# Kernel tuning notes

Hardware: AMD Instinct MI355X
Metric: run time of the kernel (lower is better)

## Reference

```python
import jax, jax.numpy as jnp
import numpy as np

NUM_HEADS = 16

def setup_inputs() -> dict:
    key = jax.random.key(0)
    ks = jax.random.split(key, 8)
    B, S, X, D = 2, 2048, 1, 1024
    scale = 1.0 / np.sqrt(D)
    return {
        "query": jax.random.normal(ks[0], (B, S, X, D), jnp.float32),
        "key": jax.random.normal(ks[1], (B, S, X, D), jnp.float32),
        "value": jax.random.normal(ks[2], (B, S, X, D), jnp.float32),
        "Wq": jax.random.normal(ks[3], (D, D), jnp.float32) * scale,
        "bq": jnp.zeros((D,), jnp.float32),
        "Wk": jax.random.normal(ks[4], (D, D), jnp.float32) * scale,
        "bk": jnp.zeros((D,), jnp.float32),
        "Wv": jax.random.normal(ks[5], (D, D), jnp.float32) * scale,
        "bv": jnp.zeros((D,), jnp.float32),
        "Wo": jax.random.normal(ks[6], (D, D), jnp.float32) * scale,
        "bo": jnp.zeros((D,), jnp.float32),
    }

def _split_heads(x, B, H):
    # [B, S, X, D] -> [B, H, S*X, depth]
    D = x.shape[-1]
    return x.reshape(B, -1, H, D // H).transpose(0, 2, 1, 3)

def reference(query, key, value, Wq, bq, Wk, bk, Wv, bv, Wo, bo):
    B, S, X, D = query.shape
    H = NUM_HEADS
    q = _split_heads(query @ Wq + bq, B, H)   # [B,H,L,dh], L=S*X
    k = _split_heads(key @ Wk + bk, B, H)
    v = _split_heads(value @ Wv + bv, B, H)
    dh = k.shape[-1]
    logits = jnp.einsum("bhqd,bhkd->bhqk", q, k) / jnp.sqrt(jnp.float32(dh))
    attn = jax.nn.softmax(logits, axis=-1)
    out = jnp.einsum("bhqk,bhkd->bhqd", attn, v)   # [B,H,L,dh]
    out = out.transpose(0, 2, 1, 3).reshape(B, S, -1, D)  # [B,S,X,D]
    return out @ Wo + bo
```

## Files before the change

### kernel.cpp

```cpp
#include <hip/hip_runtime.h>
#include <cstdint>
#include <cstddef>

typedef __bf16 bf16x8 __attribute__((ext_vector_type(8)));
typedef float f32x4 __attribute__((ext_vector_type(4)));
typedef float f32x16 __attribute__((ext_vector_type(16)));
typedef unsigned short u16;
typedef unsigned int u32;

static constexpr int Bn = 2;
static constexpr int L  = 2048;
static constexpr int Dm = 1024;
static constexpr int H  = 16;
static constexpr int DH = 64;
static constexpr int M  = Bn * L;

#define SC 0.18033688f

__device__ __forceinline__ u16 f2bf(float f) {
    union { float f; u32 u; } v; v.f = f;
    u32 u = v.u + 0x7FFFu + ((v.u >> 16) & 1u);
    return (u16)(u >> 16);
}

__device__ __forceinline__ void gl2lds16(const void* g, void* l) {
    __builtin_amdgcn_global_load_lds(
        (const __attribute__((address_space(1))) u32*)(uintptr_t)g,
        (__attribute__((address_space(3))) u32*)(uintptr_t)l, 16, 0, 0);
}

__global__ __launch_bounds__(256) void convert_in(
    const float* __restrict__ q, const float* __restrict__ k, const float* __restrict__ v,
    u16* __restrict__ dst)
{
    const float* src = (blockIdx.y == 0) ? q : (blockIdx.y == 1) ? k : v;
    u16* d = dst + (size_t)blockIdx.y * M * Dm;
    const size_t t = (size_t)blockIdx.x * 256 + threadIdx.x;
    const float4* s4 = reinterpret_cast<const float4*>(src) + t * 2;
    float4 f0 = s4[0], f1 = s4[1];
    u16 o[8] = { f2bf(f0.x), f2bf(f0.y), f2bf(f0.z), f2bf(f0.w),
                 f2bf(f1.x), f2bf(f1.y), f2bf(f1.z), f2bf(f1.w) };
    reinterpret_cast<uint4*>(d)[t] = *reinterpret_cast<uint4*>(o);
}

__global__ __launch_bounds__(256) void convert_wt(
    const float* __restrict__ Wq, const float* __restrict__ Wk,
    const float* __restrict__ Wv, const float* __restrict__ Wo,
    u16* __restrict__ dst)
{
    __shared__ u16 Ts[64][72];
    const int z = blockIdx.z;
    const float* W = (z == 0) ? Wq : (z == 1) ? Wk : (z == 2) ? Wv : Wo;
    u16* o = dst + (size_t)z * Dm * Dm;
    const int n0 = blockIdx.x * 64, k0 = blockIdx.y * 64;
    const int tid = threadIdx.x;

    {
        const int kr = tid >> 2, nc = (tid & 3) * 16;
        const float* s = W + (size_t)(k0 + kr) * Dm + n0 + nc;
        const float4* s4 = reinterpret_cast<const float4*>(s);
        float4 a = s4[0], b = s4[1], c = s4[2], d = s4[3];
        u16 t[16] = { f2bf(a.x), f2bf(a.y), f2bf(a.z), f2bf(a.w),
                      f2bf(b.x), f2bf(b.y), f2bf(b.z), f2bf(b.w),
                      f2bf(c.x), f2bf(c.y), f2bf(c.z), f2bf(c.w),
                      f2bf(d.x), f2bf(d.y), f2bf(d.z), f2bf(d.w) };
        *reinterpret_cast<uint4*>(&Ts[kr][nc])     = reinterpret_cast<uint4*>(t)[0];
        *reinterpret_cast<uint4*>(&Ts[kr][nc + 8]) = reinterpret_cast<uint4*>(t)[1];
    }
    __syncthreads();
    {
        const int nr = tid >> 2, kc = (tid & 3) * 16;
        u16 w[16];
        #pragma unroll
        for (int j = 0; j < 16; ++j) w[j] = Ts[kc + j][nr];
        u16* dptr = o + (size_t)(n0 + nr) * Dm + k0 + kc;
        *reinterpret_cast<uint4*>(dptr)     = reinterpret_cast<uint4*>(w)[0];
        *reinterpret_cast<uint4*>(dptr + 8) = reinterpret_cast<uint4*>(w)[1];
    }
}

__global__ __launch_bounds__(256) void gemm_qkv(
    const u16* __restrict__ Abuf, const u16* __restrict__ Wtb,
    const float* __restrict__ bq, const float* __restrict__ bk, const float* __restrict__ bv,
    u16* __restrict__ Qh, u16* __restrict__ Kh, u16* __restrict__ Vh)
{
    __shared__ u16 As[128 * 32];
    __shared__ u16 Bs[128 * 32];
    const int tid = threadIdx.x;
    const int wave = tid >> 6, lane = tid & 63;
    const int quad = lane >> 4, l16 = lane & 15;
    const int wr = wave >> 1, wc = wave & 1;
    const int z = blockIdx.z;
    const u16* A  = Abuf + (size_t)z * M * Dm;
    const u16* Bt = Wtb  + (size_t)z * Dm * Dm;
    const float* bias = (z == 0) ? bq : (z == 1) ? bk : bv;
    u16* out = (z == 0) ? Qh : (z == 1) ? Kh : Vh;
    const int n0 = blockIdx.x * 128, m0 = blockIdx.y * 128;

    const int srow = lane >> 2;
    const int skc  = (lane & 3) * 8;

    f32x4 acc[4][4] = {};

    for (int k0 = 0; k0 < Dm; k0 += 32) {
        __syncthreads();
        #pragma unroll
        for (int i = 0; i < 2; ++i) {
            const int ra = i * 64 + wave * 16;
            gl2lds16(A  + (size_t)(m0 + ra + srow) * Dm + k0 + skc, &As[ra * 32]);
            gl2lds16(Bt + (size_t)(n0 + ra + srow) * Dm + k0 + skc, &Bs[ra * 32]);
        }
        __syncthreads();
        bf16x8 af[4], bf[4];
        #pragma unroll
        for (int t = 0; t < 4; ++t) {
            af[t] = *reinterpret_cast<const bf16x8*>(&As[(wr * 64 + t * 16 + l16) * 32 + quad * 8]);
            bf[t] = *reinterpret_cast<const bf16x8*>(&Bs[(wc * 64 + t * 16 + l16) * 32 + quad * 8]);
        }
        #pragma unroll
        for (int mt = 0; mt < 4; ++mt)
            #pragma unroll
            for (int nt = 0; nt < 4; ++nt)
                acc[mt][nt] = __builtin_amdgcn_mfma_f32_16x16x32_bf16(af[mt], bf[nt], acc[mt][nt], 0, 0, 0);
    }

    const float qscale = (z == 0) ? SC : 1.0f;
    #pragma unroll
    for (int nt = 0; nt < 4; ++nt) {
        const int n = n0 + wc * 64 + nt * 16 + l16;
        const float badd = bias[n];
        const int h = n >> 6, d = n & 63;
        #pragma unroll
        for (int mt = 0; mt < 4; ++mt) {
            #pragma unroll
            for (int r = 0; r < 4; ++r) {
                const int m = m0 + wr * 64 + mt * 16 + quad * 4 + r;
                const int bb = m >> 11, ll = m & 2047;
                out[(((size_t)(bb * H + h)) * L + ll) * DH + d] = f2bf((acc[mt][nt][r] + badd) * qscale);
            }
        }
    }
}

__global__ __launch_bounds__(256) void transpose_v(
    const u16* __restrict__ Vh, u16* __restrict__ Vth)
{
    __shared__ u16 Ts[64][72];
    const int kt = blockIdx.x, h = blockIdx.y, b = blockIdx.z;
    const int tid = threadIdx.x;
    const size_t hb = ((size_t)(b * H + h)) * L * DH;

    {
        const int kr = tid >> 2, dc = (tid & 3) * 16;
        const u16* s = Vh + hb + (size_t)(kt * 64 + kr) * DH + dc;
        *reinterpret_cast<uint4*>(&Ts[kr][dc])     = *reinterpret_cast<const uint4*>(s);
        *reinterpret_cast<uint4*>(&Ts[kr][dc + 8]) = *reinterpret_cast<const uint4*>(s + 8);
    }
    __syncthreads();
    {
        const int dr = tid >> 2, kc = (tid & 3) * 16;
        u16 w[16];
        #pragma unroll
        for (int j = 0; j < 16; ++j) w[j] = Ts[kc + j][dr];
        u16* dptr = Vth + hb + (size_t)dr * L + kt * 64 + kc;
        *reinterpret_cast<uint4*>(dptr)     = reinterpret_cast<uint4*>(w)[0];
        *reinterpret_cast<uint4*>(dptr + 8) = reinterpret_cast<uint4*>(w)[1];
    }
}

__global__ __launch_bounds__(256) void attn(
    const u16* __restrict__ Qh, const u16* __restrict__ Kh,
    const u16* __restrict__ Vth, u16* __restrict__ ctx)
{
    __shared__ u16 KV[2 * 64 * 64];
    __shared__ u16 Os[64 * 72];

    const int tid  = threadIdx.x;
    const int wave = tid >> 6, lane = tid & 63;
    const int l31  = lane & 31, hh = lane >> 5;
    const int qt = blockIdx.x, h = blockIdx.y, b = blockIdx.z;
    const size_t hb = ((size_t)(b * H + h)) * L * DH;

    const int q0 = qt * 128 + wave * 32;

    bf16x8 qf[4];
    {
        const u16* qp = Qh + hb + (size_t)(q0 + l31) * DH + hh * 8;
        #pragma unroll
        for (int c = 0; c < 4; ++c)
            qf[c] = *reinterpret_cast<const bf16x8*>(qp + c * 16);
    }

    const int r_off = lane >> 3;
    const int s_sl  = lane & 7;

    int vbK[2], vbV[2];
    #pragma unroll
    for (int t = 0; t < 2; ++t) {
        const int rr = t * 32 + l31;
        vbK[t] = rr * 128 + ((rr & 7) << 4);
        vbV[t] = 2 * 64 * 64 + rr * 128 + ((rr & 7) << 4);
    }
    const char* ldsb = (const char*)KV;

    float rsum = 0.f;
    f32x16 oacc[2] = {};

    for (int kt = 0; kt < L / 64; ++kt) {
        __syncthreads();
        #pragma unroll
        for (int i = 0; i < 2; ++i) {
            const int rr = wave * 16 + i * 8 + r_off;
            gl2lds16(Kh  + hb + (size_t)(kt * 64 + rr) * DH + ((s_sl ^ (rr & 7)) << 3),
                     (char*)KV + (wave * 16 + i * 8) * 128);
            gl2lds16(Vth + hb + (size_t)rr * L + kt * 64 + ((s_sl ^ (rr & 7)) << 3),
                     (char*)KV + 8192 + (wave * 16 + i * 8) * 128);
        }
        __syncthreads();

        f32x16 st[2] = {};
        #pragma unroll
        for (int t = 0; t < 2; ++t) {
            #pragma unroll
            for (int c = 0; c < 4; ++c) {
                bf16x8 kf = *reinterpret_cast<const bf16x8*>(ldsb + (vbK[t] ^ (((c << 1) | hh) << 4)));
                st[t] = __builtin_amdgcn_mfma_f32_32x32x16_bf16(kf, qf[c], st[t], 0, 0, 0);
            }
        }

        bf16x8 pfrag[4];
        #pragma unroll
        for (int t = 0; t < 2; ++t) {
            float p[16];
            #pragma unroll
            for (int r = 0; r < 16; ++r) {
                p[r] = __builtin_amdgcn_exp2f(st[t][r]);
                rsum += p[r];
            }
            #pragma unroll
            for (int g = 0; g < 2; ++g) {
                float* pg = p + g * 8;
                #pragma unroll
                for (int j = 0; j < 4; ++j) {
                    asm volatile("v_permlane32_swap_b32 %0, %1" : "+v"(pg[j]), "+v"(pg[j + 4]));
                }
                u16 pk[8];
                #pragma unroll
                for (int j = 0; j < 8; ++j) pk[j] = f2bf(pg[j]);
                pfrag[t * 2 + g] = *reinterpret_cast<bf16x8*>(pk);
            }
        }

        #pragma unroll
        for (int t = 0; t < 2; ++t) {
            #pragma unroll
            for (int c = 0; c < 4; ++c) {
                bf16x8 vf = *reinterpret_cast<const bf16x8*>(ldsb + (vbV[t] ^ (((c << 1) | hh) << 4)));
                oacc[t] = __builtin_amdgcn_mfma_f32_32x32x16_bf16(vf, pfrag[c], oacc[t], 0, 0, 0);
            }
        }
    }

    rsum += __shfl_xor(rsum, 32);
    const float inv = 1.0f / rsum;

    for (int pass = 0; pass < 2; ++pass) {
        __syncthreads();
        if ((wave >> 1) == pass) {
            const int qloc = (wave & 1) * 32 + l31;
            #pragma unroll
            for (int t = 0; t < 2; ++t)
                #pragma unroll
                for (int r = 0; r < 16; ++r) {
                    const int d = t * 32 + (r & 3) + ((r >> 2) << 3) + hh * 4;
                    Os[qloc * 72 + d] = f2bf(oacc[t][r] * inv);
                }
        }
        __syncthreads();
        {
            const int row = tid >> 2, cc = (tid & 3) * 16;
            u16* dst = ctx + ((size_t)(b * L + qt * 128 + pass * 64 + row)) * Dm + h * 64 + cc;
            *reinterpret_cast<uint4*>(dst)     = *reinterpret_cast<const uint4*>(&Os[row * 72 + cc]);
            *reinterpret_cast<uint4*>(dst + 8) = *reinterpret_cast<const uint4*>(&Os[row * 72 + cc + 8]);
        }
    }
}

__global__ __launch_bounds__(256) void gemm_out(
    const u16* __restrict__ A, const u16* __restrict__ Bt,
    const float* __restrict__ bias, float* __restrict__ out)
{
    __shared__ u16 As[128 * 32];
    __shared__ u16 Bs[64 * 32];
    const int tid = threadIdx.x;
    const int wave = tid >> 6, lane = tid & 63;
    const int quad = lane >> 4, l16 = lane & 15;
    const int n0 = blockIdx.x * 64, m0 = blockIdx.y * 128;

    const int srow = lane >> 2;
    const int skc  = (lane & 3) * 8;

    f32x4 acc[2][4] = {};

    for (int k0 = 0; k0 < Dm; k0 += 32) {
        __syncthreads();
        #pragma unroll
        for (int i = 0; i < 2; ++i) {
            const int ra = i * 64 + wave * 16;
            gl2lds16(A + (size_t)(m0 + ra + srow) * Dm + k0 + skc, &As[ra * 32]);
        }
        gl2lds16(Bt + (size_t)(n0 + wave * 16 + srow) * Dm + k0 + skc, &Bs[wave * 16 * 32]);
        __syncthreads();
        bf16x8 af[2], bf[4];
        #pragma unroll
        for (int t = 0; t < 2; ++t)
            af[t] = *reinterpret_cast<const bf16x8*>(&As[(wave * 32 + t * 16 + l16) * 32 + quad * 8]);
        #pragma unroll
        for (int t = 0; t < 4; ++t)
            bf[t] = *reinterpret_cast<const bf16x8*>(&Bs[(t * 16 + l16) * 32 + quad * 8]);
        #pragma unroll
        for (int mt = 0; mt < 2; ++mt)
            #pragma unroll
            for (int nt = 0; nt < 4; ++nt)
                acc[mt][nt] = __builtin_amdgcn_mfma_f32_16x16x32_bf16(af[mt], bf[nt], acc[mt][nt], 0, 0, 0);
    }

    #pragma unroll
    for (int nt = 0; nt < 4; ++nt) {
        const int n = n0 + nt * 16 + l16;
        const float badd = bias[n];
        #pragma unroll
        for (int mt = 0; mt < 2; ++mt) {
            #pragma unroll
            for (int r = 0; r < 4; ++r) {
                const int m = m0 + wave * 32 + mt * 16 + quad * 4 + r;
                out[(size_t)m * Dm + n] = acc[mt][nt][r] + badd;
            }
        }
    }
}

extern "C" void kernel_launch(void* const* d_in, const int* in_sizes, int n_in,
                              void* d_out, int out_size, void* d_ws, size_t ws_size,
                              hipStream_t stream) {
    const float* q  = (const float*)d_in[0];
    const float* k  = (const float*)d_in[1];
    const float* v  = (const float*)d_in[2];
    const float* Wq = (const float*)d_in[3];
    const float* bq = (const float*)d_in[4];
    const float* Wk = (const float*)d_in[5];
    const float* bk = (const float*)d_in[6];
    const float* Wv = (const float*)d_in[7];
    const float* bv = (const float*)d_in[8];
    const float* Wo = (const float*)d_in[9];
    const float* bo = (const float*)d_in[10];
    float* out = (float*)d_out;

    const size_t per = (size_t)Bn * H * L * DH;
    u16* Abuf = (u16*)d_ws;
    u16* Wt   = Abuf + 3 * (size_t)M * Dm;
    u16* Qh   = Wt + 4 * (size_t)Dm * Dm;
    u16* Kh   = Qh + per;
    u16* Vh   = Kh + per;
    u16* Vth  = Vh + per;
    u16* ctx  = Abuf;

    convert_in <<<dim3((M * Dm) / 8 / 256, 3), 256, 0, stream>>>(q, k, v, Abuf);
    convert_wt <<<dim3(Dm / 64, Dm / 64, 4), 256, 0, stream>>>(Wq, Wk, Wv, Wo, Wt);
    gemm_qkv   <<<dim3(Dm / 128, M / 128, 3), 256, 0, stream>>>(Abuf, Wt, bq, bk, bv, Qh, Kh, Vh);
    transpose_v<<<dim3(L / 64, H, Bn), 256, 0, stream>>>(Vh, Vth);
    attn       <<<dim3(L / 128, H, Bn), 256, 0, stream>>>(Qh, Kh, Vth, ctx);
    gemm_out   <<<dim3(Dm / 64, M / 128), 256, 0, stream>>>(ctx, Wt + 3 * (size_t)Dm * Dm, bo, out);
}
```

Baseline: 239.0 us.

## Fuse V transpose into QKV GEMM, split attention KV across 8 waves, pack bf16 converts

The QKV GEMM epilogue now writes V directly in transposed layout, so the separate transpose_v kernel and its extra global round-trip are gone. The attention kernel moves to 512 threads: two groups of four waves each process alternate 64-key tiles and merge partial outputs and row sums through LDS at the end. This halves the serial KV loop length per wave. Scalar float-to-bf16 conversions are replaced with a packed conversion builtin where available. The trade-offs are higher LDS use, an extra reduction phase, and strided 4-byte stores for the transposed V writes.

```diff
diff --git a/kernel.cpp b/kernel.cpp
--- a/kernel.cpp
+++ b/kernel.cpp
@@ -23,6 +23,17 @@
     return (u16)(u >> 16);
 }
 
+__device__ __forceinline__ u32 pk_bf16(float a, float b) {
+#if __has_builtin(__builtin_amdgcn_cvt_pk_bf16_f32)
+    typedef __bf16 bf16x2_t __attribute__((ext_vector_type(2)));
+    bf16x2_t t = __builtin_amdgcn_cvt_pk_bf16_f32(a, b);
+    u32 r; __builtin_memcpy(&r, &t, 4); return r;
+#else
+    return (u32)f2bf(a) | ((u32)f2bf(b) << 16);
+#endif
+}
+__device__ __forceinline__ u16 f2bf1(float f) { return (u16)(pk_bf16(f, f) & 0xffffu); }
+
 __device__ __forceinline__ void gl2lds16(const void* g, void* l) {
     __builtin_amdgcn_global_load_lds(
         (const __attribute__((address_space(1))) u32*)(uintptr_t)g,
@@ -38,8 +49,8 @@
     const size_t t = (size_t)blockIdx.x * 256 + threadIdx.x;
     const float4* s4 = reinterpret_cast<const float4*>(src) + t * 2;
     float4 f0 = s4[0], f1 = s4[1];
-    u16 o[8] = { f2bf(f0.x), f2bf(f0.y), f2bf(f0.z), f2bf(f0.w),
-                 f2bf(f1.x), f2bf(f1.y), f2bf(f1.z), f2bf(f1.w) };
+    u32 o[4] = { pk_bf16(f0.x, f0.y), pk_bf16(f0.z, f0.w),
+                 pk_bf16(f1.x, f1.y), pk_bf16(f1.z, f1.w) };
     reinterpret_cast<uint4*>(d)[t] = *reinterpret_cast<uint4*>(o);
 }
 
@@ -60,10 +71,8 @@
         const float* s = W + (size_t)(k0 + kr) * Dm + n0 + nc;
         const float4* s4 = reinterpret_cast<const float4*>(s);
         float4 a = s4[0], b = s4[1], c = s4[2], d = s4[3];
-        u16 t[16] = { f2bf(a.x), f2bf(a.y), f2bf(a.z), f2bf(a.w),
-                      f2bf(b.x), f2bf(b.y), f2bf(b.z), f2bf(b.w),
-                      f2bf(c.x), f2bf(c.y), f2bf(c.z), f2bf(c.w),
-                      f2bf(d.x), f2bf(d.y), f2bf(d.z), f2bf(d.w) };
+        u32 t[8] = { pk_bf16(a.x, a.y), pk_bf16(a.z, a.w), pk_bf16(b.x, b.y), pk_bf16(b.z, b.w),
+                     pk_bf16(c.x, c.y), pk_bf16(c.z, c.w), pk_bf16(d.x, d.y), pk_bf16(d.z, d.w) };
         *reinterpret_cast<uint4*>(&Ts[kr][nc])     = reinterpret_cast<uint4*>(t)[0];
         *reinterpret_cast<uint4*>(&Ts[kr][nc + 8]) = reinterpret_cast<uint4*>(t)[1];
     }
@@ -82,7 +91,7 @@
 __global__ __launch_bounds__(256) void gemm_qkv(
     const u16* __restrict__ Abuf, const u16* __restrict__ Wtb,
     const float* __restrict__ bq, const float* __restrict__ bk, const float* __restrict__ bv,
-    u16* __restrict__ Qh, u16* __restrict__ Kh, u16* __restrict__ Vh)
+    u16* __restrict__ Qh, u16* __restrict__ Kh, u16* __restrict__ Vth)
 {
     __shared__ u16 As[128 * 32];
     __shared__ u16 Bs[128 * 32];
@@ -94,7 +103,7 @@
     const u16* A  = Abuf + (size_t)z * M * Dm;
     const u16* Bt = Wtb  + (size_t)z * Dm * Dm;
     const float* bias = (z == 0) ? bq : (z == 1) ? bk : bv;
-    u16* out = (z == 0) ? Qh : (z == 1) ? Kh : Vh;
+    u16* out = (z == 0) ? Qh : (z == 1) ? Kh : Vth;
     const int n0 = blockIdx.x * 128, m0 = blockIdx.y * 128;
 
     const int srow = lane >> 2;
@@ -132,56 +141,39 @@
         const int h = n >> 6, d = n & 63;
         #pragma unroll
         for (int mt = 0; mt < 4; ++mt) {
-            #pragma unroll
-            for (int r = 0; r < 4; ++r) {
-                const int m = m0 + wr * 64 + mt * 16 + quad * 4 + r;
-                const int bb = m >> 11, ll = m & 2047;
-                out[(((size_t)(bb * H + h)) * L + ll) * DH + d] = f2bf((acc[mt][nt][r] + badd) * qscale);
-            }
-        }
-    }
-}
-
-__global__ __launch_bounds__(256) void transpose_v(
-    const u16* __restrict__ Vh, u16* __restrict__ Vth)
-{
-    __shared__ u16 Ts[64][72];
-    const int kt = blockIdx.x, h = blockIdx.y, b = blockIdx.z;
-    const int tid = threadIdx.x;
-    const size_t hb = ((size_t)(b * H + h)) * L * DH;
-
-    {
-        const int kr = tid >> 2, dc = (tid & 3) * 16;
-        const u16* s = Vh + hb + (size_t)(kt * 64 + kr) * DH + dc;
-        *reinterpret_cast<uint4*>(&Ts[kr][dc])     = *reinterpret_cast<const uint4*>(s);
-        *reinterpret_cast<uint4*>(&Ts[kr][dc + 8]) = *reinterpret_cast<const uint4*>(s + 8);
-    }
-    __syncthreads();
-    {
-        const int dr = tid >> 2, kc = (tid & 3) * 16;
-        u16 w[16];
-        #pragma unroll
-        for (int j = 0; j < 16; ++j) w[j] = Ts[kc + j][dr];
-        u16* dptr = Vth + hb + (size_t)dr * L + kt * 64 + kc;
-        *reinterpret_cast<uint4*>(dptr)     = reinterpret_cast<uint4*>(w)[0];
-        *reinterpret_cast<uint4*>(dptr + 8) = reinterpret_cast<uint4*>(w)[1];
-    }
-}
-
-__global__ __launch_bounds__(256) void attn(
+            const int mb = m0 + wr * 64 + mt * 16 + quad * 4;
+            const int bb = mb >> 11, ll = mb & 2047;
+            if (z == 2) {
+                u16* vp = out + (((size_t)(bb * H + h)) * DH + d) * L + ll;
+                *reinterpret_cast<u32*>(vp)     = pk_bf16(acc[mt][nt][0] + badd, acc[mt][nt][1] + badd);
+                *reinterpret_cast<u32*>(vp + 2) = pk_bf16(acc[mt][nt][2] + badd, acc[mt][nt][3] + badd);
+            } else {
+                #pragma unroll
+                for (int r = 0; r < 4; ++r)
+                    out[(((size_t)(bb * H + h)) * L + ll + r) * DH + d] =
+                        f2bf1((acc[mt][nt][r] + badd) * qscale);
+            }
+        }
+    }
+}
+
+__global__ __launch_bounds__(512) void attn(
     const u16* __restrict__ Qh, const u16* __restrict__ Kh,
     const u16* __restrict__ Vth, u16* __restrict__ ctx)
 {
-    __shared__ u16 KV[2 * 64 * 64];
-    __shared__ u16 Os[64 * 72];
+    __shared__ __align__(16) char smem[45056];
+    u16* Os = (u16*)(smem + 35840);
+    float* rsums = (float*)(smem + 34816);
 
     const int tid  = threadIdx.x;
-    const int wave = tid >> 6, lane = tid & 63;
+    const int w    = tid >> 6, lane = tid & 63;
     const int l31  = lane & 31, hh = lane >> 5;
     const int qt = blockIdx.x, h = blockIdx.y, b = blockIdx.z;
     const size_t hb = ((size_t)(b * H + h)) * L * DH;
 
-    const int q0 = qt * 128 + wave * 32;
+    const int qsub  = w & 3;
+    const int mybuf = w >> 2;
+    const int q0 = qt * 128 + qsub * 32;
 
     bf16x8 qf[4];
     {
@@ -191,30 +183,35 @@
             qf[c] = *reinterpret_cast<const bf16x8*>(qp + c * 16);
     }
 
-    const int r_off = lane >> 3;
-    const int s_sl  = lane & 7;
-
+    char* stbase = smem + (w >> 2) * 16384 + ((w >> 1) & 1) * 8192;
+    const bool st_isK = ((w >> 1) & 1) == 0;
+    const int row_half = (w & 1) * 32;
+    const int rlane = lane >> 3;
+    const int s_sw  = (lane & 7) ^ rlane;
+
+    const char* ldsb = smem + mybuf * 16384;
     int vbK[2], vbV[2];
     #pragma unroll
     for (int t = 0; t < 2; ++t) {
         const int rr = t * 32 + l31;
         vbK[t] = rr * 128 + ((rr & 7) << 4);
-        vbV[t] = 2 * 64 * 64 + rr * 128 + ((rr & 7) << 4);
-    }
-    const char* ldsb = (const char*)KV;
+        vbV[t] = 8192 + rr * 128 + ((rr & 7) << 4);
+    }
 
     float rsum = 0.f;
     f32x16 oacc[2] = {};
 
-    for (int kt = 0; kt < L / 64; ++kt) {
-        __syncthreads();
-        #pragma unroll
-        for (int i = 0; i < 2; ++i) {
-            const int rr = wave * 16 + i * 8 + r_off;
-            gl2lds16(Kh  + hb + (size_t)(kt * 64 + rr) * DH + ((s_sl ^ (rr & 7)) << 3),
-                     (char*)KV + (wave * 16 + i * 8) * 128);
-            gl2lds16(Vth + hb + (size_t)rr * L + kt * 64 + ((s_sl ^ (rr & 7)) << 3),
-                     (char*)KV + 8192 + (wave * 16 + i * 8) * 128);
+    for (int r = 0; r < L / 128; ++r) {
+        const int tile = 2 * r + mybuf;
+        const int stile = 2 * r + (w >> 2);
+        __syncthreads();
+        #pragma unroll
+        for (int i = 0; i < 4; ++i) {
+            const int rloc = row_half + i * 8 + rlane;
+            const void* src = st_isK
+                ? (const void*)(Kh  + hb + (size_t)(stile * 64 + rloc) * DH + s_sw * 8)
+                : (const void*)(Vth + hb + (size_t)rloc * L + stile * 64 + s_sw * 8);
+            gl2lds16(src, stbase + (row_half + i * 8) * 128);
         }
         __syncthreads();
 
@@ -233,21 +230,20 @@
         for (int t = 0; t < 2; ++t) {
             float p[16];
             #pragma unroll
-            for (int r = 0; r < 16; ++r) {
-                p[r] = __builtin_amdgcn_exp2f(st[t][r]);
-                rsum += p[r];
+            for (int rr = 0; rr < 16; ++rr) {
+                p[rr] = __builtin_amdgcn_exp2f(st[t][rr]);
+                rsum += p[rr];
             }
             #pragma unroll
             for (int g = 0; g < 2; ++g) {
                 float* pg = p + g * 8;
                 #pragma unroll
-                for (int j = 0; j < 4; ++j) {
+                for (int j = 0; j < 4; ++j)
                     asm volatile("v_permlane32_swap_b32 %0, %1" : "+v"(pg[j]), "+v"(pg[j + 4]));
-                }
-                u16 pk[8];
+                u32 pkv[4];
                 #pragma unroll
-                for (int j = 0; j < 8; ++j) pk[j] = f2bf(pg[j]);
-                pfrag[t * 2 + g] = *reinterpret_cast<bf16x8*>(pk);
+                for (int j = 0; j < 4; ++j) pkv[j] = pk_bf16(pg[2 * j], pg[2 * j + 1]);
+                pfrag[t * 2 + g] = *reinterpret_cast<bf16x8*>(pkv);
             }
         }
 
@@ -261,27 +257,49 @@
         }
     }
 
-    rsum += __shfl_xor(rsum, 32);
-    const float inv = 1.0f / rsum;
-
+    __syncthreads();
+    float* mb = (float*)smem + (size_t)qsub * 2176 + lane * 34;
+    if (w >= 4) {
+        #pragma unroll
+        for (int t = 0; t < 2; ++t)
+            #pragma unroll
+            for (int rr = 0; rr < 16; ++rr) mb[t * 16 + rr] = oacc[t][rr];
+        rsums[qsub * 64 + lane] = rsum;
+    }
+    __syncthreads();
+    float inv = 0.f;
+    if (w < 4) {
+        #pragma unroll
+        for (int t = 0; t < 2; ++t)
+            #pragma unroll
+            for (int rr = 0; rr < 16; ++rr) oacc[t][rr] += mb[t * 16 + rr];
+        rsum += rsums[qsub * 64 + lane];
+        rsum += __shfl_xor(rsum, 32);
+        inv = 1.0f / rsum;
+    }
+
+    #pragma unroll
     for (int pass = 0; pass < 2; ++pass) {
         __syncthreads();
-        if ((wave >> 1) == pass) {
-            const int qloc = (wave & 1) * 32 + l31;
-            #pragma unroll
-            for (int t = 0; t < 2; ++t)
+        if ((w >> 1) == pass) {
+            const int qloc = (w & 1) * 32 + l31;
+            #pragma unroll
+            for (int t = 0; t < 2; ++t) {
                 #pragma unroll
-                for (int r = 0; r < 16; ++r) {
-                    const int d = t * 32 + (r & 3) + ((r >> 2) << 3) + hh * 4;
-                    Os[qloc * 72 + d] = f2bf(oacc[t][r] * inv);
+                for (int rq = 0; rq < 4; ++rq) {
+                    const int d0 = t * 32 + rq * 8 + hh * 4;
+                    *reinterpret_cast<u32*>(&Os[qloc * 72 + d0]) =
+                        pk_bf16(oacc[t][rq * 4 + 0] * inv, oacc[t][rq * 4 + 1] * inv);
+                    *reinterpret_cast<u32*>(&Os[qloc * 72 + d0 + 2]) =
+                        pk_bf16(oacc[t][rq * 4 + 2] * inv, oacc[t][rq * 4 + 3] * inv);
                 }
+            }
         }
         __syncthreads();
         {
-            const int row = tid >> 2, cc = (tid & 3) * 16;
+            const int row = tid >> 3, cc = (tid & 7) * 8;
             u16* dst = ctx + ((size_t)(b * L + qt * 128 + pass * 64 + row)) * Dm + h * 64 + cc;
-            *reinterpret_cast<uint4*>(dst)     = *reinterpret_cast<const uint4*>(&Os[row * 72 + cc]);
-            *reinterpret_cast<uint4*>(dst + 8) = *reinterpret_cast<const uint4*>(&Os[row * 72 + cc + 8]);
+            *reinterpret_cast<uint4*>(dst) = *reinterpret_cast<const uint4*>(&Os[row * 72 + cc]);
         }
     }
 }
@@ -361,14 +379,12 @@
     u16* Wt   = Abuf + 3 * (size_t)M * Dm;
     u16* Qh   = Wt + 4 * (size_t)Dm * Dm;
     u16* Kh   = Qh + per;
-    u16* Vh   = Kh + per;
-    u16* Vth  = Vh + per;
+    u16* Vth  = Kh + per;
     u16* ctx  = Abuf;
 
     convert_in <<<dim3((M * Dm) / 8 / 256, 3), 256, 0, stream>>>(q, k, v, Abuf);
     convert_wt <<<dim3(Dm / 64, Dm / 64, 4), 256, 0, stream>>>(Wq, Wk, Wv, Wo, Wt);
-    gemm_qkv   <<<dim3(Dm / 128, M / 128, 3), 256, 0, stream>>>(Abuf, Wt, bq, bk, bv, Qh, Kh, Vh);
-    transpose_v<<<dim3(L / 64, H, Bn), 256, 0, stream>>>(Vh, Vth);
-    attn       <<<dim3(L / 128, H, Bn), 256, 0, stream>>>(Qh, Kh, Vth, ctx);
+    gemm_qkv   <<<dim3(Dm / 128, M / 128, 3), 256, 0, stream>>>(Abuf, Wt, bq, bk, bv, Qh, Kh, Vth);
+    attn       <<<dim3(L / 128, H, Bn), 512, 0, stream>>>(Qh, Kh, Vth, ctx);
     gemm_out   <<<dim3(Dm / 64, M / 128), 256, 0, stream>>>(ctx, Wt + 3 * (size_t)Dm * Dm, bo, out);
 }
```

Result: slower. 264.0 us (+10.4%).
